# Optimization experiments

Measured on AMD Instinct MI355X. Metric: run time of the kernel, lower is better.

Reference implementation:

```python
import jax, jax.numpy as jnp
import numpy as np

B, C, H, W = 4, 256, 64, 64


def setup_inputs() -> dict:
    key = jax.random.key(0)
    k1, k2, k3, k4 = jax.random.split(key, 4)
    inp = jax.random.normal(k1, (B, C, H, W), dtype=jnp.float32)
    inter_mask = jnp.ones((B, 1, H, W), dtype=jnp.float32)
    flow_init = jax.random.normal(k2, (B, 2, H, W), dtype=jnp.float32)
    # nn.Linear(C, C): weight [out,in], bias [out]
    lim = 1.0 / np.sqrt(C)
    W_lin = jax.random.uniform(k3, (C, C), dtype=jnp.float32, minval=-lim, maxval=lim)
    b_lin = jax.random.uniform(k4, (C,), dtype=jnp.float32, minval=-lim, maxval=lim)
    return {"inp": inp, "inter_mask": inter_mask, "flow_init": flow_init,
            "W_lin": W_lin, "b_lin": b_lin}


def reference(inp, inter_mask, flow_init, W_lin, b_lin):
    batch, ch, ht, wd = inp.shape
    n = ht * wd
    # [B, N, C]
    x = inp.reshape(batch, ch, n).transpose(0, 2, 1)
    x = x @ W_lin.T + b_lin
    scale = ch ** (-0.5)
    # [B, N, N] full self-correlation
    scores = jnp.einsum('bnc,bmc->bnm', x * scale, x)
    attn = jax.nn.softmax(scores, axis=-1)
    # [B, N, 2]
    flow = flow_init.reshape(batch, 2, n).transpose(0, 2, 1)
    flow_add = attn @ flow
    # [B, 2, H, W]
    return flow_add.reshape(batch, ht, wd, 2).transpose(0, 3, 1, 2)
```

## Files before the change

### kernel.cpp

```cpp
#include <hip/hip_runtime.h>
#include <hip/hip_bf16.h>

#define NB 4
#define CCH 256
#define NN 4096
#define QT 256
#define KSPLIT 8
#define MRANGE (NN / KSPLIT)
#define MTILE 64
#define NTILES (MRANGE / MTILE)
#define VPAD 8

#define SQRTK 0.30028060f

typedef __attribute__((ext_vector_type(8))) short short8;
typedef __attribute__((ext_vector_type(16))) float f32x16;
typedef __attribute__((ext_vector_type(4))) int i32x4;

__device__ inline ushort f2bf(float f) {
    uint u = __float_as_uint(f);
    uint r = (u + 0x7fffu + ((u >> 16) & 1u)) >> 16;
    return (ushort)r;
}

__device__ inline float dev_exp2(float x) {
#if __has_builtin(__builtin_amdgcn_exp2f)
    return __builtin_amdgcn_exp2f(x);
#else
    return exp2f(x);
#endif
}

__device__ inline void gl_lds16(const void* g, void* l) {
    __builtin_amdgcn_global_load_lds(
        (const __attribute__((address_space(1))) unsigned int*)g,
        (__attribute__((address_space(3))) unsigned int*)l, 16, 0, 0);
}

__global__ void wconv_k(const float* __restrict__ W, ushort* __restrict__ Wb) {
    int i = blockIdx.x * 256 + threadIdx.x;
    float4 v = reinterpret_cast<const float4*>(W)[i];
    ushort4 r;
    r.x = f2bf(v.x); r.y = f2bf(v.y); r.z = f2bf(v.z); r.w = f2bf(v.w);
    reinterpret_cast<ushort4*>(Wb)[i] = r;
}

__global__ __launch_bounds__(256) void fusedlin_k(const float* __restrict__ inp,
                                                  const ushort* __restrict__ Wb,
                                                  const float* __restrict__ bias,
                                                  ushort* __restrict__ xs) {
    int wg = blockIdx.x;
    int b = wg >> 6, nt = wg & 63;
    int t = threadIdx.x, l = t & 63, w = t >> 6;
    __shared__ float ftile[64 * 67];
    __shared__ ushort xtile[64][260];

    for (int cblk = 0; cblk < 4; cblk++) {
        const float* src = inp + ((size_t)(b * CCH + cblk * 64)) * NN + nt * 64;
#pragma unroll
        for (int p = 0; p < 4; p++) {
            int ci = p * 256 + t;
            int c = ci >> 4, n4 = ci & 15;
            float4 v = *reinterpret_cast<const float4*>(src + (size_t)c * NN + n4 * 4);
            float* d = &ftile[c * 67 + n4 * 4];
            d[0] = v.x; d[1] = v.y; d[2] = v.z; d[3] = v.w;
        }
        __syncthreads();
#pragma unroll
        for (int p = 0; p < 2; p++) {
            int u = p * 256 + t;
            int n = u >> 3, cc = u & 7;
            ushort tmp[8];
#pragma unroll
            for (int j = 0; j < 8; j++) tmp[j] = f2bf(ftile[(cc * 8 + j) * 67 + n]);
            uint4 o;
            o.x = (uint)tmp[0] | ((uint)tmp[1] << 16);
            o.y = (uint)tmp[2] | ((uint)tmp[3] << 16);
            o.z = (uint)tmp[4] | ((uint)tmp[5] << 16);
            o.w = (uint)tmp[6] | ((uint)tmp[7] << 16);
            *reinterpret_cast<uint4*>(&xtile[n][cblk * 64 + cc * 8]) = o;
        }
        __syncthreads();
    }

    int nb = (w & 1) * 32;
    int obase = (w >> 1) * 128;
    const ushort* wrow = Wb + ((size_t)(obase + (l & 31))) * CCH + ((l >> 5) * 8);
    f32x16 acc[4];
#pragma unroll
    for (int os = 0; os < 4; os++)
#pragma unroll
        for (int r = 0; r < 16; r++) acc[os][r] = 0.f;

    const char* arow = (const char*)&xtile[nb + (l & 31)][0] + (l >> 5) * 16;
#pragma unroll
    for (int ch = 0; ch < 16; ch++) {
        short8 a = *reinterpret_cast<const short8*>(arow + ch * 32);
#pragma unroll
        for (int os = 0; os < 4; os++) {
            short8 bb = *reinterpret_cast<const short8*>(wrow + (size_t)os * 32 * CCH + ch * 16);
            acc[os] = __builtin_amdgcn_mfma_f32_32x32x16_bf16(a, bb, acc[os], 0, 0, 0);
        }
    }
#pragma unroll
    for (int os = 0; os < 4; os++) {
        int oc = obase + os * 32 + (l & 31);
        float bv = bias[oc];
#pragma unroll
        for (int r = 0; r < 16; r++) {
            int row = (r & 3) + 8 * (r >> 2) + 4 * (l >> 5);
            float v = (acc[os][r] + bv) * SQRTK;
            xs[((size_t)(b * NN + nt * 64 + nb + row)) * CCH + oc] = f2bf(v);
        }
    }
}

__global__ __launch_bounds__(256, 2) void attn_k(const ushort* __restrict__ xs,
                                                 const float* __restrict__ flow,
                                                 float* __restrict__ part) {
    int wg = blockIdx.x;
    int b = wg >> 7;
    int qt = (wg >> 3) & 15;
    int ks = wg & 7;
    int t = threadIdx.x, l = t & 63, w = t >> 6;
    const ushort* xb = xs + (size_t)b * NN * CCH;
    int qbase = qt * QT + w * 64;
    int mstart = ks * MRANGE;

    __shared__ ushort kt[2][MTILE * 256];
    __shared__ ushort vlds[4][MRANGE + VPAD];

    {
        int m0 = t * 2;
        float2 fx2 = *reinterpret_cast<const float2*>(flow + (size_t)b * 2 * NN + mstart + m0);
        float2 fy2 = *reinterpret_cast<const float2*>(flow + (size_t)b * 2 * NN + NN + mstart + m0);
        float fxv[2] = {fx2.x, fx2.y};
        float fyv[2] = {fy2.x, fy2.y};
#pragma unroll
        for (int i = 0; i < 2; i++) {
            int m = m0 + i, ml = m & 15;
            int pos = (m & ~15) | (ml & 3) | ((ml & 4) << 1) | ((ml & 8) >> 1);
            vlds[0][pos] = f2bf(fxv[i]);
            vlds[1][pos] = f2bf(fyv[i]);
            vlds[2][pos] = 0x3F80;
            vlds[3][pos] = 0;
        }
    }

    short8 qf0[16], qf1[16];
    const ushort* qrow0 = xb + ((size_t)(qbase + (l & 31))) * CCH + (l >> 5) * 8;
    const ushort* qrow1 = qrow0 + (size_t)32 * CCH;
#pragma unroll
    for (int ch = 0; ch < 16; ch++) {
        qf0[ch] = *reinterpret_cast<const short8*>(qrow0 + ch * 16);
        qf1[ch] = *reinterpret_cast<const short8*>(qrow1 + ch * 16);
    }

    f32x16 pv0, pv1;
#pragma unroll
    for (int r = 0; r < 16; r++) { pv0[r] = 0.f; pv1[r] = 0.f; }

    auto stage = [&](int buf, int tile) {
        int mb = mstart + tile * MTILE;
        const char* src = (const char*)(xb + (size_t)mb * CCH);
#pragma unroll
        for (int p = 0; p < 8; p++) {
            int chunk = w * 8 + p;
            int lin = chunk * 1024 + l * 16;
            int row = lin >> 9;
            int cb = lin & 511;
            int gsw = cb ^ ((row & 15) << 4);
            gl_lds16(src + (size_t)row * 512 + gsw, &kt[buf][chunk * 512]);
        }
    };

    int c_sel = (l & 31) < 3 ? (l & 31) : 3;
    stage(0, 0);
    __syncthreads();
    int cur = 0;
    for (int tile = 0; tile < NTILES; tile++) {
        if (tile + 1 < NTILES) stage(cur ^ 1, tile + 1);
#pragma unroll
        for (int ms = 0; ms < 2; ms++) {
            f32x16 S0, S1;
#pragma unroll
            for (int r = 0; r < 16; r++) { S0[r] = 0.f; S1[r] = 0.f; }
            const char* base = (const char*)&kt[cur][(ms * 32 + (l & 31)) * 256];
            int swz = (l & 15) << 4;
#pragma unroll
            for (int ch = 0; ch < 16; ch++) {
                int cbyte = (ch * 32 + ((l >> 5) * 16)) ^ swz;
                short8 kf = *reinterpret_cast<const short8*>(base + cbyte);
                S0 = __builtin_amdgcn_mfma_f32_32x32x16_bf16(kf, qf0[ch], S0, 0, 0, 0);
                S1 = __builtin_amdgcn_mfma_f32_32x32x16_bf16(kf, qf1[ch], S1, 0, 0, 0);
            }
#pragma unroll
            for (int r = 0; r < 16; r++) { S0[r] = dev_exp2(S0[r]); S1[r] = dev_exp2(S1[r]); }
            uint wa[8], wb2[8];
#pragma unroll
            for (int p = 0; p < 8; p++) {
                asm("v_cvt_pk_bf16_f32 %0, %1, %2" : "=v"(wa[p]) : "v"(S0[2 * p]), "v"(S0[2 * p + 1]));
                asm("v_cvt_pk_bf16_f32 %0, %1, %2" : "=v"(wb2[p]) : "v"(S1[2 * p]), "v"(S1[2 * p + 1]));
            }
            i32x4 a0 = {(int)wa[0], (int)wa[1], (int)wa[2], (int)wa[3]};
            i32x4 a1 = {(int)wa[4], (int)wa[5], (int)wa[6], (int)wa[7]};
            i32x4 b0 = {(int)wb2[0], (int)wb2[1], (int)wb2[2], (int)wb2[3]};
            i32x4 b1 = {(int)wb2[4], (int)wb2[5], (int)wb2[6], (int)wb2[7]};
            short8 pa00 = __builtin_bit_cast(short8, a0);
            short8 pa01 = __builtin_bit_cast(short8, a1);
            short8 pa10 = __builtin_bit_cast(short8, b0);
            short8 pa11 = __builtin_bit_cast(short8, b1);
            int mloc = tile * MTILE + ms * 32;
            const ushort* vb = &vlds[c_sel][mloc + (l >> 5) * 8];
            short8 v0 = *reinterpret_cast<const short8*>(vb);
            short8 v1 = *reinterpret_cast<const short8*>(vb + 16);
            pv0 = __builtin_amdgcn_mfma_f32_32x32x16_bf16(pa00, v0, pv0, 0, 0, 0);
            pv0 = __builtin_amdgcn_mfma_f32_32x32x16_bf16(pa01, v1, pv0, 0, 0, 0);
            pv1 = __builtin_amdgcn_mfma_f32_32x32x16_bf16(pa10, v0, pv1, 0, 0, 0);
            pv1 = __builtin_amdgcn_mfma_f32_32x32x16_bf16(pa11, v1, pv1, 0, 0, 0);
        }
        __syncthreads();
        cur ^= 1;
    }

    int c = l & 31;
    if (c < 3) {
        float* pb = part + ((size_t)(b * KSPLIT + ks)) * 3 * NN;
        int off = ((c + 1) % 3) * NN;
#pragma unroll
        for (int r = 0; r < 16; r++) {
            int row = (r & 3) + 8 * (r >> 2) + 4 * (l >> 5);
            pb[off + qbase + row] = pv0[r];
            pb[off + qbase + 32 + row] = pv1[r];
        }
    }
}

__global__ void finalize_k(const float* __restrict__ part, float* __restrict__ out) {
    int i = blockIdx.x * 256 + threadIdx.x;
    int b = i >> 12, n = i & 4095;
    float s = 0.f, x = 0.f, y = 0.f;
#pragma unroll
    for (int ks = 0; ks < KSPLIT; ks++) {
        const float* p = part + ((size_t)(b * KSPLIT + ks)) * 3 * NN;
        s += p[n];
        x += p[NN + n];
        y += p[2 * NN + n];
    }
    out[(size_t)b * 2 * NN + n] = x / s;
    out[(size_t)b * 2 * NN + NN + n] = y / s;
}

extern "C" void kernel_launch(void* const* d_in, const int* in_sizes, int n_in,
                              void* d_out, int out_size, void* d_ws, size_t ws_size,
                              hipStream_t stream) {
    const float* inp  = (const float*)d_in[0];
    const float* flow = (const float*)d_in[2];
    const float* W    = (const float*)d_in[3];
    const float* bias = (const float*)d_in[4];
    float* out = (float*)d_out;

    char* ws = (char*)d_ws;
    ushort* xs   = (ushort*)(ws);
    float*  part = (float*)(ws + 8388608);
    ushort* Wb   = (ushort*)(ws + 16777216);

    wconv_k<<<64, 256, 0, stream>>>(W, Wb);
    fusedlin_k<<<256, 256, 0, stream>>>(inp, Wb, bias, xs);
    attn_k<<<512, 256, 0, stream>>>(xs, flow, part);
    finalize_k<<<64, 256, 0, stream>>>(part, out);
}
```

Baseline: 67.01 us.

## Shrink query tile per wave and halve key split in attention kernel

The attention kernel now gives each wave 32 queries instead of 64 and splits the key range 4 ways instead of 8. Each wave processes both 32-key halves of a 64-key tile with a single Q fragment, which halves Q register use and the partial-sum writes to the finalize pass. The trade-off is that K tiles in LDS are reused across fewer queries, so each wave needs more LDS reads per MFMA. The linear-projection kernel also moves to 32-row tiles over 512 workgroups to raise parallelism. The lower register pressure may allow better occupancy.

```diff
diff --git a/kernel.cpp b/kernel.cpp
--- a/kernel.cpp
+++ b/kernel.cpp
@@ -4,8 +4,8 @@
 #define NB 4
 #define CCH 256
 #define NN 4096
-#define QT 256
-#define KSPLIT 8
+#define QT 128
+#define KSPLIT 4
 #define MRANGE (NN / KSPLIT)
 #define MTILE 64
 #define NTILES (MRANGE / MTILE)
@@ -50,29 +50,27 @@
                                                   const float* __restrict__ bias,
                                                   ushort* __restrict__ xs) {
     int wg = blockIdx.x;
-    int b = wg >> 6, nt = wg & 63;
+    int b = wg >> 7, nt = wg & 127;
     int t = threadIdx.x, l = t & 63, w = t >> 6;
-    __shared__ float ftile[64 * 67];
-    __shared__ ushort xtile[64][260];
+    __shared__ float ftile[64 * 33];
+    __shared__ ushort xtile[32][260];
 
     for (int cblk = 0; cblk < 4; cblk++) {
-        const float* src = inp + ((size_t)(b * CCH + cblk * 64)) * NN + nt * 64;
-#pragma unroll
-        for (int p = 0; p < 4; p++) {
+        const float* src = inp + ((size_t)(b * CCH + cblk * 64)) * NN + nt * 32;
+#pragma unroll
+        for (int p = 0; p < 2; p++) {
             int ci = p * 256 + t;
-            int c = ci >> 4, n4 = ci & 15;
+            int c = ci >> 3, n4 = ci & 7;
             float4 v = *reinterpret_cast<const float4*>(src + (size_t)c * NN + n4 * 4);
-            float* d = &ftile[c * 67 + n4 * 4];
+            float* d = &ftile[c * 33 + n4 * 4];
             d[0] = v.x; d[1] = v.y; d[2] = v.z; d[3] = v.w;
         }
         __syncthreads();
-#pragma unroll
-        for (int p = 0; p < 2; p++) {
-            int u = p * 256 + t;
-            int n = u >> 3, cc = u & 7;
+        {
+            int n = t >> 3, cc = t & 7;
             ushort tmp[8];
 #pragma unroll
-            for (int j = 0; j < 8; j++) tmp[j] = f2bf(ftile[(cc * 8 + j) * 67 + n]);
+            for (int j = 0; j < 8; j++) tmp[j] = f2bf(ftile[(cc * 8 + j) * 33 + n]);
             uint4 o;
             o.x = (uint)tmp[0] | ((uint)tmp[1] << 16);
             o.y = (uint)tmp[2] | ((uint)tmp[3] << 16);
@@ -83,34 +81,33 @@
         __syncthreads();
     }
 
-    int nb = (w & 1) * 32;
-    int obase = (w >> 1) * 128;
+    int obase = w * 64;
     const ushort* wrow = Wb + ((size_t)(obase + (l & 31))) * CCH + ((l >> 5) * 8);
-    f32x16 acc[4];
-#pragma unroll
-    for (int os = 0; os < 4; os++)
+    f32x16 acc[2];
+#pragma unroll
+    for (int os = 0; os < 2; os++)
 #pragma unroll
         for (int r = 0; r < 16; r++) acc[os][r] = 0.f;
 
-    const char* arow = (const char*)&xtile[nb + (l & 31)][0] + (l >> 5) * 16;
+    const char* arow = (const char*)&xtile[l & 31][0] + (l >> 5) * 16;
 #pragma unroll
     for (int ch = 0; ch < 16; ch++) {
         short8 a = *reinterpret_cast<const short8*>(arow + ch * 32);
 #pragma unroll
-        for (int os = 0; os < 4; os++) {
+        for (int os = 0; os < 2; os++) {
             short8 bb = *reinterpret_cast<const short8*>(wrow + (size_t)os * 32 * CCH + ch * 16);
             acc[os] = __builtin_amdgcn_mfma_f32_32x32x16_bf16(a, bb, acc[os], 0, 0, 0);
         }
     }
 #pragma unroll
-    for (int os = 0; os < 4; os++) {
+    for (int os = 0; os < 2; os++) {
         int oc = obase + os * 32 + (l & 31);
         float bv = bias[oc];
 #pragma unroll
         for (int r = 0; r < 16; r++) {
             int row = (r & 3) + 8 * (r >> 2) + 4 * (l >> 5);
             float v = (acc[os][r] + bv) * SQRTK;
-            xs[((size_t)(b * NN + nt * 64 + nb + row)) * CCH + oc] = f2bf(v);
+            xs[((size_t)(b * NN + nt * 32 + row)) * CCH + oc] = f2bf(v);
         }
     }
 }
@@ -120,24 +117,24 @@
                                                  float* __restrict__ part) {
     int wg = blockIdx.x;
     int b = wg >> 7;
-    int qt = (wg >> 3) & 15;
-    int ks = wg & 7;
+    int qt = (wg >> 2) & 31;
+    int ks = wg & 3;
     int t = threadIdx.x, l = t & 63, w = t >> 6;
     const ushort* xb = xs + (size_t)b * NN * CCH;
-    int qbase = qt * QT + w * 64;
+    int qbase = qt * QT + w * 32;
     int mstart = ks * MRANGE;
 
     __shared__ ushort kt[2][MTILE * 256];
     __shared__ ushort vlds[4][MRANGE + VPAD];
 
     {
-        int m0 = t * 2;
-        float2 fx2 = *reinterpret_cast<const float2*>(flow + (size_t)b * 2 * NN + mstart + m0);
-        float2 fy2 = *reinterpret_cast<const float2*>(flow + (size_t)b * 2 * NN + NN + mstart + m0);
-        float fxv[2] = {fx2.x, fx2.y};
-        float fyv[2] = {fy2.x, fy2.y};
-#pragma unroll
-        for (int i = 0; i < 2; i++) {
+        int m0 = t * 4;
+        float4 fx4 = *reinterpret_cast<const float4*>(flow + (size_t)b * 2 * NN + mstart + m0);
+        float4 fy4 = *reinterpret_cast<const float4*>(flow + (size_t)b * 2 * NN + NN + mstart + m0);
+        float fxv[4] = {fx4.x, fx4.y, fx4.z, fx4.w};
+        float fyv[4] = {fy4.x, fy4.y, fy4.z, fy4.w};
+#pragma unroll
+        for (int i = 0; i < 4; i++) {
             int m = m0 + i, ml = m & 15;
             int pos = (m & ~15) | (ml & 3) | ((ml & 4) << 1) | ((ml & 8) >> 1);
             vlds[0][pos] = f2bf(fxv[i]);
@@ -147,18 +144,15 @@
         }
     }
 
-    short8 qf0[16], qf1[16];
-    const ushort* qrow0 = xb + ((size_t)(qbase + (l & 31))) * CCH + (l >> 5) * 8;
-    const ushort* qrow1 = qrow0 + (size_t)32 * CCH;
-#pragma unroll
-    for (int ch = 0; ch < 16; ch++) {
-        qf0[ch] = *reinterpret_cast<const short8*>(qrow0 + ch * 16);
-        qf1[ch] = *reinterpret_cast<const short8*>(qrow1 + ch * 16);
-    }
-
-    f32x16 pv0, pv1;
-#pragma unroll
-    for (int r = 0; r < 16; r++) { pv0[r] = 0.f; pv1[r] = 0.f; }
+    short8 qf[16];
+    const ushort* qrow = xb + ((size_t)(qbase + (l & 31))) * CCH + (l >> 5) * 8;
+#pragma unroll
+    for (int ch = 0; ch < 16; ch++)
+        qf[ch] = *reinterpret_cast<const short8*>(qrow + ch * 16);
+
+    f32x16 pv;
+#pragma unroll
+    for (int r = 0; r < 16; r++) pv[r] = 0.f;
 
     auto stage = [&](int buf, int tile) {
         int mb = mstart + tile * MTILE;
@@ -180,45 +174,48 @@
     int cur = 0;
     for (int tile = 0; tile < NTILES; tile++) {
         if (tile + 1 < NTILES) stage(cur ^ 1, tile + 1);
-#pragma unroll
-        for (int ms = 0; ms < 2; ms++) {
-            f32x16 S0, S1;
-#pragma unroll
-            for (int r = 0; r < 16; r++) { S0[r] = 0.f; S1[r] = 0.f; }
-            const char* base = (const char*)&kt[cur][(ms * 32 + (l & 31)) * 256];
-            int swz = (l & 15) << 4;
-#pragma unroll
-            for (int ch = 0; ch < 16; ch++) {
-                int cbyte = (ch * 32 + ((l >> 5) * 16)) ^ swz;
-                short8 kf = *reinterpret_cast<const short8*>(base + cbyte);
-                S0 = __builtin_amdgcn_mfma_f32_32x32x16_bf16(kf, qf0[ch], S0, 0, 0, 0);
-                S1 = __builtin_amdgcn_mfma_f32_32x32x16_bf16(kf, qf1[ch], S1, 0, 0, 0);
-            }
-#pragma unroll
-            for (int r = 0; r < 16; r++) { S0[r] = dev_exp2(S0[r]); S1[r] = dev_exp2(S1[r]); }
-            uint wa[8], wb2[8];
-#pragma unroll
-            for (int p = 0; p < 8; p++) {
-                asm("v_cvt_pk_bf16_f32 %0, %1, %2" : "=v"(wa[p]) : "v"(S0[2 * p]), "v"(S0[2 * p + 1]));
-                asm("v_cvt_pk_bf16_f32 %0, %1, %2" : "=v"(wb2[p]) : "v"(S1[2 * p]), "v"(S1[2 * p + 1]));
-            }
-            i32x4 a0 = {(int)wa[0], (int)wa[1], (int)wa[2], (int)wa[3]};
-            i32x4 a1 = {(int)wa[4], (int)wa[5], (int)wa[6], (int)wa[7]};
-            i32x4 b0 = {(int)wb2[0], (int)wb2[1], (int)wb2[2], (int)wb2[3]};
-            i32x4 b1 = {(int)wb2[4], (int)wb2[5], (int)wb2[6], (int)wb2[7]};
-            short8 pa00 = __builtin_bit_cast(short8, a0);
-            short8 pa01 = __builtin_bit_cast(short8, a1);
-            short8 pa10 = __builtin_bit_cast(short8, b0);
-            short8 pa11 = __builtin_bit_cast(short8, b1);
-            int mloc = tile * MTILE + ms * 32;
-            const ushort* vb = &vlds[c_sel][mloc + (l >> 5) * 8];
-            short8 v0 = *reinterpret_cast<const short8*>(vb);
-            short8 v1 = *reinterpret_cast<const short8*>(vb + 16);
-            pv0 = __builtin_amdgcn_mfma_f32_32x32x16_bf16(pa00, v0, pv0, 0, 0, 0);
-            pv0 = __builtin_amdgcn_mfma_f32_32x32x16_bf16(pa01, v1, pv0, 0, 0, 0);
-            pv1 = __builtin_amdgcn_mfma_f32_32x32x16_bf16(pa10, v0, pv1, 0, 0, 0);
-            pv1 = __builtin_amdgcn_mfma_f32_32x32x16_bf16(pa11, v1, pv1, 0, 0, 0);
-        }
+        f32x16 S0, S1;
+#pragma unroll
+        for (int r = 0; r < 16; r++) { S0[r] = 0.f; S1[r] = 0.f; }
+        const char* base0 = (const char*)&kt[cur][(l & 31) * 256];
+        const char* base1 = (const char*)&kt[cur][(32 + (l & 31)) * 256];
+        int swz = (l & 15) << 4;
+#pragma unroll
+        for (int ch = 0; ch < 16; ch++) {
+            int cbyte = (ch * 32 + ((l >> 5) * 16)) ^ swz;
+            short8 kf0 = *reinterpret_cast<const short8*>(base0 + cbyte);
+            short8 kf1 = *reinterpret_cast<const short8*>(base1 + cbyte);
+            S0 = __builtin_amdgcn_mfma_f32_32x32x16_bf16(kf0, qf[ch], S0, 0, 0, 0);
+            S1 = __builtin_amdgcn_mfma_f32_32x32x16_bf16(kf1, qf[ch], S1, 0, 0, 0);
+        }
+#pragma unroll
+        for (int r = 0; r < 16; r++) { S0[r] = dev_exp2(S0[r]); S1[r] = dev_exp2(S1[r]); }
+        uint wa[8], wb2[8];
+#pragma unroll
+        for (int p = 0; p < 8; p++) {
+            asm("v_cvt_pk_bf16_f32 %0, %1, %2" : "=v"(wa[p]) : "v"(S0[2 * p]), "v"(S0[2 * p + 1]));
+            asm("v_cvt_pk_bf16_f32 %0, %1, %2" : "=v"(wb2[p]) : "v"(S1[2 * p]), "v"(S1[2 * p + 1]));
+        }
+        i32x4 a0 = {(int)wa[0], (int)wa[1], (int)wa[2], (int)wa[3]};
+        i32x4 a1 = {(int)wa[4], (int)wa[5], (int)wa[6], (int)wa[7]};
+        i32x4 b0 = {(int)wb2[0], (int)wb2[1], (int)wb2[2], (int)wb2[3]};
+        i32x4 b1 = {(int)wb2[4], (int)wb2[5], (int)wb2[6], (int)wb2[7]};
+        short8 pa00 = __builtin_bit_cast(short8, a0);
+        short8 pa01 = __builtin_bit_cast(short8, a1);
+        short8 pa10 = __builtin_bit_cast(short8, b0);
+        short8 pa11 = __builtin_bit_cast(short8, b1);
+        int mloc0 = tile * MTILE;
+        int mloc1 = tile * MTILE + 32;
+        const ushort* vb0 = &vlds[c_sel][mloc0 + (l >> 5) * 8];
+        const ushort* vb1 = &vlds[c_sel][mloc1 + (l >> 5) * 8];
+        short8 v00 = *reinterpret_cast<const short8*>(vb0);
+        short8 v01 = *reinterpret_cast<const short8*>(vb0 + 16);
+        short8 v10 = *reinterpret_cast<const short8*>(vb1);
+        short8 v11 = *reinterpret_cast<const short8*>(vb1 + 16);
+        pv = __builtin_amdgcn_mfma_f32_32x32x16_bf16(pa00, v00, pv, 0, 0, 0);
+        pv = __builtin_amdgcn_mfma_f32_32x32x16_bf16(pa01, v01, pv, 0, 0, 0);
+        pv = __builtin_amdgcn_mfma_f32_32x32x16_bf16(pa10, v10, pv, 0, 0, 0);
+        pv = __builtin_amdgcn_mfma_f32_32x32x16_bf16(pa11, v11, pv, 0, 0, 0);
         __syncthreads();
         cur ^= 1;
     }
@@ -230,8 +227,7 @@
 #pragma unroll
         for (int r = 0; r < 16; r++) {
             int row = (r & 3) + 8 * (r >> 2) + 4 * (l >> 5);
-            pb[off + qbase + row] = pv0[r];
-            pb[off + qbase + 32 + row] = pv1[r];
+            pb[off + qbase + row] = pv[r];
         }
     }
 }
@@ -266,7 +262,7 @@
     ushort* Wb   = (ushort*)(ws + 16777216);
 
     wconv_k<<<64, 256, 0, stream>>>(W, Wb);
-    fusedlin_k<<<256, 256, 0, stream>>>(inp, Wb, bias, xs);
+    fusedlin_k<<<512, 256, 0, stream>>>(inp, Wb, bias, xs);
     attn_k<<<512, 256, 0, stream>>>(xs, flow, part);
     finalize_k<<<64, 256, 0, stream>>>(part, out);
 }
```

Measured after the change: 67.62 us. No clear change (+0.9%).
